# Kernel optimization log

Measured on AMD Instinct MI355X. Metric: run time of the kernel, lower is better.

The kernel has to match this reference:

```python
import jax, jax.numpy as jnp
import numpy as np

N = 50000
E = 800000
D_IN, D_HID, D_OUT = 128, 128, 128
BN_EPS = 1e-5


def gcn_conv(x, W, b, src, dst, n_nodes):
    # PyG GCNConv: add self-loops, symmetric normalization, scatter-add aggregation.
    loop = jnp.arange(n_nodes)
    s = jnp.concatenate([src, loop])
    d = jnp.concatenate([dst, loop])
    w = jnp.ones(s.shape[0], x.dtype)
    deg = jax.ops.segment_sum(w, d, num_segments=n_nodes)
    dinv = jnp.where(deg > 0, jax.lax.rsqrt(deg), 0.0)
    norm = dinv[s] * w * dinv[d]            # [E+N]
    h = x @ W                                # [N, d_out]
    msg = norm[:, None] * h[s]               # gather + scale
    out = jax.ops.segment_sum(msg, d, num_segments=n_nodes)
    return out + b


def batchnorm_prelu(x, gamma, beta, alpha):
    # BatchNorm1d in training mode (batch statistics, biased variance) + PReLU.
    mu = jnp.mean(x, axis=0)
    var = jnp.mean(jnp.square(x - mu), axis=0)
    y = (x - mu) * jax.lax.rsqrt(var + BN_EPS) * gamma + beta
    return jnp.where(y > 0, y, alpha * y)


def setup_inputs() -> dict:
    key = jax.random.key(0)
    ks = jax.random.split(key, 4)
    x = jax.random.normal(ks[0], (N, D_IN), dtype=jnp.float32)
    edge_index = jax.random.randint(ks[1], (2, E), 0, N, dtype=jnp.int64)
    s1 = 1.0 / np.sqrt(D_IN)
    s2 = 1.0 / np.sqrt(D_HID)
    W1 = jax.random.uniform(ks[2], (D_IN, D_HID), jnp.float32, -s1, s1)
    W2 = jax.random.uniform(ks[3], (D_HID, D_OUT), jnp.float32, -s2, s2)
    return {
        "x": x,
        "edge_index": edge_index,
        "W1": W1, "b1": jnp.zeros((D_HID,), jnp.float32),
        "g1": jnp.ones((D_HID,), jnp.float32), "be1": jnp.zeros((D_HID,), jnp.float32),
        "a1": jnp.full((1,), 0.25, jnp.float32),
        "W2": W2, "b2": jnp.zeros((D_OUT,), jnp.float32),
        "g2": jnp.ones((D_OUT,), jnp.float32), "be2": jnp.zeros((D_OUT,), jnp.float32),
        "a2": jnp.full((1,), 0.25, jnp.float32),
    }


def reference(x, edge_index, W1, b1, g1, be1, a1, W2, b2, g2, be2, a2):
    src, dst = edge_index[0], edge_index[1]
    h = gcn_conv(x, W1, b1, src, dst, N)
    h = batchnorm_prelu(h, g1, be1, a1)
    h = gcn_conv(h, W2, b2, src, dst, N)
    h = batchnorm_prelu(h, g2, be2, a2)
    return h
```

## Files before the change

kernel.cpp:

```cpp
#include <hip/hip_runtime.h>
#include <hip/hip_bf16.h>


typedef __hip_bfloat16 bf16;
typedef __attribute__((ext_vector_type(8))) short short8;
typedef __attribute__((ext_vector_type(4))) float f32x4;

#define NN 50000
#define NE 800000
#define DD 128
#define BN_EPS 1e-5f
#define BIN_CHUNK 3125
#define CAP 18432
#define NBKT 49

__device__ __forceinline__ float b2f(bf16 v) { return __bfloat162float(v); }
__device__ __forceinline__ float ldf(const void* p, size_t idx, int isbf) {
  return isbf ? b2f(((const bf16*)p)[idx]) : ((const float*)p)[idx];
}
__device__ __forceinline__ int lde(const void* ei, size_t idx, int is64) {
  return is64 ? (int)((const long long*)ei)[idx] : ((const int*)ei)[idx];
}
__device__ __forceinline__ unsigned int f2bs(float v) {
  bf16 b = __float2bfloat16(v);
  return (unsigned int)*reinterpret_cast<unsigned short*>(&b);
}
__device__ __forceinline__ float bslo(unsigned int u) { return __uint_as_float(u << 16); }
__device__ __forceinline__ float bshi(unsigned int u) { return __uint_as_float(u & 0xFFFF0000u); }
__device__ __forceinline__ float s2f(short v) {
  return __uint_as_float(((unsigned int)(unsigned short)v) << 16);
}

__global__ __launch_bounds__(256) void k_bin(const int* ei_i, const unsigned short* x16,
                                             const void* W1, const void* W2,
                                             unsigned short* wp1, unsigned short* wp2,
                                             int* flags, int* tailc, unsigned int* binned) {
  __shared__ int cnt[64], cur[64], gb[64], sflags[2];
  __shared__ unsigned int ebuf[BIN_CHUNK];
  const int tid = threadIdx.x;
  const int bid = blockIdx.x;
  if (tid < 64) {
    unsigned long long m1 = __ballot(ei_i[2 * tid + 1] != 0);
    int ex = (x16[2 * tid] >> 7) & 0xFF;
    unsigned long long m2 = __ballot(ex >= 90 && ex <= 140);
    if (tid == 0) {
      sflags[0] = (m1 == 0ull) ? 1 : 0;
      sflags[1] = (__popcll(m2) >= 48) ? 1 : 0;
    }
    cnt[tid] = 0;
    cur[tid] = 0;
  }
  __syncthreads();
  const int is64 = sflags[0], isbf = sflags[1];
  if (bid == 0 && tid == 0) { flags[0] = is64; flags[1] = isbf; }
  if (bid < 128) {
    const void* W = bid < 64 ? W1 : W2;
    unsigned short* wp = bid < 64 ? wp1 : wp2;
    int idx = (bid & 63) * 256 + tid;
    int k = idx >> 7, n = idx & 127;
    wp[(k >> 3) * 1024 + n * 8 + (k & 7)] = (unsigned short)f2bs(ldf(W, idx, isbf));
  }
  const void* ei = (const void*)ei_i;
  const int e0 = bid * BIN_CHUNK;
  for (int t = tid; t < BIN_CHUNK; t += 256) {
    int s = lde(ei, (size_t)(e0 + t), is64);
    int d = lde(ei, (size_t)NE + e0 + t, is64);
    ebuf[t] = ((unsigned)s << 16) | ((unsigned)(d >> 10) << 10) | (unsigned)(d & 1023);
    atomicAdd(&cnt[d >> 10], 1);
  }
  __syncthreads();
  if (tid < 64 && cnt[tid] > 0) gb[tid] = tid * CAP + atomicAdd(&tailc[tid], cnt[tid]);
  __syncthreads();
  for (int t = tid; t < BIN_CHUNK; t += 256) {
    unsigned int u = ebuf[t];
    int b = (int)((u >> 10) & 63);
    int r = atomicAdd(&cur[b], 1);
    binned[gb[b] + r] = u;
  }
}

__global__ __launch_bounds__(1024) void k_degfill(const unsigned int* binned, const int* tailc,
                                                  float* dinv, int* rowptr, int* rowend,
                                                  int* csr_src) {
  __shared__ int hist[1024];
  const int b = blockIdx.x;
  const int t = threadIdx.x;
  hist[t] = 0;
  __syncthreads();
  const int eb = b * CAP, ee = eb + tailc[b];
  for (int e = eb + t; e < ee; e += 1024) atomicAdd(&hist[binned[e] & 1023], 1);
  __syncthreads();
  int h = hist[t];
  __syncthreads();
  for (int off = 1; off < 1024; off <<= 1) {
    int u = (t >= off) ? hist[t - off] : 0;
    __syncthreads();
    hist[t] += u;
    __syncthreads();
  }
  int start = eb + hist[t] - h;
  int node = b * 1024 + t;
  if (node < NN) {
    rowptr[node] = start;
    rowend[node] = start + h;
    dinv[node] = rsqrtf((float)(h + 1));
  }
  __syncthreads();
  hist[t] = start;
  __syncthreads();
  for (int e = eb + t; e < ee; e += 1024) {
    unsigned int u = binned[e];
    int pos = atomicAdd(&hist[u & 1023], 1);
    csr_src[pos] = (int)(u >> 16);
  }
}

template <int XMODE>
__global__ __launch_bounds__(256) void k_gemm(const void* in_, const unsigned short* wp,
                                              const int* flags, const float* dinv,
                                              const float* statsp, const void* g,
                                              const void* be, const void* al,
                                              float* zstats, unsigned int* out) {
  __shared__ alignas(16) short sW[16 * 128 * 8];
  __shared__ float sSc[DD], sSh[DD], sAl;
  const int isbf = flags[1];
  const int tid = threadIdx.x;

  if (blockIdx.x < 64) zstats[blockIdx.x * 256 + tid] = 0.f;
  {
    const short8* src = (const short8*)wp;
    short8* dst = (short8*)sW;
#pragma unroll
    for (int i = 0; i < 8; i++) dst[tid + i * 256] = src[tid + i * 256];
  }
  if (XMODE == 2) {
    if (tid < DD) {
      float s = 0.f, q = 0.f;
#pragma unroll 8
      for (int k = 0; k < 64; k++) {
        s += statsp[k * 256 + tid];
        q += statsp[k * 256 + 128 + tid];
      }
      const float inv_n = 1.0f / NN;
      float mu = s * inv_n;
      float var = q * inv_n - mu * mu;
      float sc = rsqrtf(var + BN_EPS) * ldf(g, tid, isbf);
      sSc[tid] = sc;
      sSh[tid] = ldf(be, tid, isbf) - mu * sc;
    }
    if (tid == 0) sAl = ldf(al, 0, isbf);
  }
  __syncthreads();

  const int wave = tid >> 6;
  const int lane = tid & 63;
  const int quad = lane >> 4;
  const int m16 = lane & 15;
  const int r0 = blockIdx.x * 128 + wave * 32;

  f32x4 acc[2][8];
#pragma unroll
  for (int t = 0; t < 2; t++)
#pragma unroll
    for (int n = 0; n < 8; n++) acc[t][n] = (f32x4){0.f, 0.f, 0.f, 0.f};

#pragma unroll
  for (int q = 0; q < 4; q++) {
    const int kq = q * 32 + quad * 8;
    short8 af[2];
#pragma unroll
    for (int t = 0; t < 2; t++) {
      int row = r0 + t * 16 + m16;
      row = row < NN ? row : NN - 1;
      if (XMODE == 2) {
        short8 raw = *(const short8*)((const short*)in_ + (size_t)row * DD + kq);
        short8 f;
#pragma unroll
        for (int jj = 0; jj < 8; jj++) {
          float y = s2f(raw[jj]);
          y = y * sSc[kq + jj] + sSh[kq + jj];
          y = y > 0.f ? y : sAl * y;
          f[jj] = (short)f2bs(y);
        }
        af[t] = f;
      } else if (isbf) {
        af[t] = *(const short8*)((const short*)in_ + (size_t)row * DD + kq);
      } else {
        const float* ap = (const float*)in_ + (size_t)row * DD + kq;
        const float4 u0 = *(const float4*)ap;
        const float4 u1 = *(const float4*)(ap + 4);
        float v[8] = {u0.x, u0.y, u0.z, u0.w, u1.x, u1.y, u1.z, u1.w};
        short8 f;
#pragma unroll
        for (int jj = 0; jj < 8; jj++) f[jj] = (short)f2bs(v[jj]);
        af[t] = f;
      }
    }
    const int c = q * 4 + quad;
    const short* bp = sW + c * 1024 + m16 * 8;
#pragma unroll
    for (int n = 0; n < 8; n++) {
      const short8 bfrag = *(const short8*)(bp + n * 128);
      acc[0][n] = __builtin_amdgcn_mfma_f32_16x16x32_bf16(af[0], bfrag, acc[0][n], 0, 0, 0);
      acc[1][n] = __builtin_amdgcn_mfma_f32_16x16x32_bf16(af[1], bfrag, acc[1][n], 0, 0, 0);
    }
  }

#pragma unroll
  for (int t = 0; t < 2; t++)
#pragma unroll
    for (int r = 0; r < 4; r++) {
      int row = r0 + t * 16 + quad * 4 + r;
      if (row < NN) {
        float di = dinv[row];
        unsigned int* orow = out + (size_t)row * 64;
#pragma unroll
        for (int n = 0; n < 4; n++) {
          unsigned int p = (f2bs(di * acc[t][n + 4][r]) << 16) | f2bs(di * acc[t][n][r]);
          orow[n * 16 + m16] = p;
        }
      }
    }
}

__global__ __launch_bounds__(256) void k_agg(const unsigned int* hs, const float* dinv,
                                             const int* rowptr, const int* rowend,
                                             const int* csr_src, const void* bias,
                                             const int* flags, unsigned short* out,
                                             float* statsp) {
  const int tid = threadIdx.x;
  int w = (blockIdx.x * 256 + tid) >> 6;
  int lane = tid & 63;
  float dd_ = dinv[w];
  unsigned int hv = hs[(size_t)w * 64 + lane];
  float ax = bslo(hv), ay = bshi(hv);
  int e = rowptr[w], e1 = rowend[w];
  for (; e + 7 < e1; e += 8) {
    int s0 = csr_src[e], s1 = csr_src[e + 1], s2 = csr_src[e + 2], s3 = csr_src[e + 3];
    int s4 = csr_src[e + 4], s5 = csr_src[e + 5], s6 = csr_src[e + 6], s7 = csr_src[e + 7];
    unsigned int v0 = hs[(size_t)s0 * 64 + lane];
    unsigned int v1 = hs[(size_t)s1 * 64 + lane];
    unsigned int v2 = hs[(size_t)s2 * 64 + lane];
    unsigned int v3 = hs[(size_t)s3 * 64 + lane];
    unsigned int v4 = hs[(size_t)s4 * 64 + lane];
    unsigned int v5 = hs[(size_t)s5 * 64 + lane];
    unsigned int v6 = hs[(size_t)s6 * 64 + lane];
    unsigned int v7 = hs[(size_t)s7 * 64 + lane];
    ax += bslo(v0) + bslo(v1) + bslo(v2) + bslo(v3) + bslo(v4) + bslo(v5) + bslo(v6) + bslo(v7);
    ay += bshi(v0) + bshi(v1) + bshi(v2) + bshi(v3) + bshi(v4) + bshi(v5) + bshi(v6) + bshi(v7);
  }
  for (; e + 3 < e1; e += 4) {
    int s0 = csr_src[e], s1 = csr_src[e + 1], s2 = csr_src[e + 2], s3 = csr_src[e + 3];
    unsigned int v0 = hs[(size_t)s0 * 64 + lane];
    unsigned int v1 = hs[(size_t)s1 * 64 + lane];
    unsigned int v2 = hs[(size_t)s2 * 64 + lane];
    unsigned int v3 = hs[(size_t)s3 * 64 + lane];
    ax += bslo(v0) + bslo(v1) + bslo(v2) + bslo(v3);
    ay += bshi(v0) + bshi(v1) + bshi(v2) + bshi(v3);
  }
  for (; e < e1; e++) {
    unsigned int v0 = hs[(size_t)csr_src[e] * 64 + lane];
    ax += bslo(v0);
    ay += bshi(v0);
  }
  int isbf = flags[1];
  float o1 = dd_ * ax + ldf(bias, lane, isbf);
  float o2 = dd_ * ay + ldf(bias, lane + 64, isbf);
  unsigned short* orow = out + (size_t)w * DD;
  orow[lane] = (unsigned short)f2bs(o1);
  orow[lane + 64] = (unsigned short)f2bs(o2);

  __shared__ float rs1[256], rq1[256], rs2[256], rq2[256];
  rs1[tid] = o1; rq1[tid] = o1 * o1;
  rs2[tid] = o2; rq2[tid] = o2 * o2;
  __syncthreads();
  float* p = statsp + (blockIdx.x & 63) * 256;
  if (tid < 64) {
    float s = rs1[tid] + rs1[tid + 64] + rs1[tid + 128] + rs1[tid + 192];
    float q = rq1[tid] + rq1[tid + 64] + rq1[tid + 128] + rq1[tid + 192];
    atomicAdd(&p[tid], s);
    atomicAdd(&p[128 + tid], q);
  } else if (tid < 128) {
    int l = tid - 64;
    float s = rs2[l] + rs2[l + 64] + rs2[l + 128] + rs2[l + 192];
    float q = rq2[l] + rq2[l + 64] + rq2[l + 128] + rq2[l + 192];
    atomicAdd(&p[tid], s);
    atomicAdd(&p[128 + tid], q);
  }
}

__global__ __launch_bounds__(256) void k_bn_apply(const unsigned int* x32, const float* statsp,
                                                  const void* g, const void* be, const void* al,
                                                  const int* flags, void* out) {
  __shared__ float sSc[DD], sSh[DD], sAl;
  const int tid = threadIdx.x;
  const int isbf = flags[1];
  if (tid < DD) {
    float s = 0.f, q = 0.f;
#pragma unroll 8
    for (int k = 0; k < 64; k++) {
      s += statsp[k * 256 + tid];
      q += statsp[k * 256 + 128 + tid];
    }
    const float inv_n = 1.0f / NN;
    float mu = s * inv_n;
    float var = q * inv_n - mu * mu;
    float sc = rsqrtf(var + BN_EPS) * ldf(g, tid, isbf);
    sSc[tid] = sc;
    sSh[tid] = ldf(be, tid, isbf) - mu * sc;
  }
  if (tid == 0) sAl = ldf(al, 0, isbf);
  __syncthreads();
  const float alpha = sAl;
  for (int i4 = blockIdx.x * 256 + tid; i4 < NN * 32; i4 += gridDim.x * 256) {
    int jq = (i4 & 31) * 4;
    const uint2 xv = ((const uint2*)x32)[i4];
    float xa[4] = {bslo(xv.x), bshi(xv.x), bslo(xv.y), bshi(xv.y)};
    float y[4];
#pragma unroll
    for (int u = 0; u < 4; u++) {
      int j = jq + u;
      float v = xa[u] * sSc[j] + sSh[j];
      y[u] = v > 0.f ? v : alpha * v;
    }
    if (isbf) {
      uint2 o;
      o.x = (f2bs(y[1]) << 16) | f2bs(y[0]);
      o.y = (f2bs(y[3]) << 16) | f2bs(y[2]);
      ((uint2*)out)[i4] = o;
    } else {
      float4 o = {y[0], y[1], y[2], y[3]};
      ((float4*)out)[i4] = o;
    }
  }
}

extern "C" void kernel_launch(void* const* d_in, const int* in_sizes, int n_in,
                              void* d_out, int out_size, void* d_ws, size_t ws_size,
                              hipStream_t stream) {
  const void* x = d_in[0];
  const int* ei = (const int*)d_in[1];
  const void* W1 = d_in[2];
  const void* b1 = d_in[3];
  const void* g1 = d_in[4];
  const void* be1 = d_in[5];
  const void* a1 = d_in[6];
  const void* W2 = d_in[7];
  const void* b2 = d_in[8];
  const void* g2 = d_in[9];
  const void* be2 = d_in[10];
  const void* a2 = d_in[11];

  char* w = (char*)d_ws;
  float* dinv = (float*)w;
  int* flags = (int*)(w + 200704);
  int* rowptr = (int*)(w + 404800);
  int* rowend = (int*)(w + 604816);
  int* tailc = (int*)(w + 805632);
  float* stats1p = (float*)(w + 806400);
  float* stats2p = (float*)(w + 871936);
  int* csr_src = (int*)(w + 1048576);
  unsigned int* hbuf = (unsigned int*)(w + 4718592);
  unsigned short* wp1 = (unsigned short*)(w + 17518592);
  unsigned short* wp2 = (unsigned short*)(w + 17551360);
  unsigned short* aggbuf = (unsigned short*)(w + 30056448);
  unsigned int* binned = (unsigned int*)(w + 42856448);

  const int NB_G = (NN + 127) / 128;
  const int NB_W = NN * 64 / 256;

  hipMemsetAsync(tailc, 0, 256, stream);
  k_bin<<<dim3(256), dim3(256), 0, stream>>>(ei, (const unsigned short*)x, W1, W2,
                                             wp1, wp2, flags, tailc, binned);
  k_degfill<<<dim3(NBKT), dim3(1024), 0, stream>>>(binned, tailc, dinv, rowptr, rowend,
                                                   csr_src);

  k_gemm<0><<<dim3(NB_G), dim3(256), 0, stream>>>(x, wp1, flags, dinv,
                                                  nullptr, nullptr, nullptr, nullptr,
                                                  stats1p, hbuf);
  k_agg<<<dim3(NB_W), dim3(256), 0, stream>>>(hbuf, dinv, rowptr, rowend, csr_src,
                                              b1, flags, aggbuf, stats1p);

  k_gemm<2><<<dim3(NB_G), dim3(256), 0, stream>>>(aggbuf, wp2, flags, dinv,
                                                  stats1p, g1, be1, a1, stats2p, hbuf);
  k_agg<<<dim3(NB_W), dim3(256), 0, stream>>>(hbuf, dinv, rowptr, rowend, csr_src,
                                              b2, flags, aggbuf, stats2p);
  k_bn_apply<<<dim3(1024), dim3(256), 0, stream>>>((const unsigned int*)aggbuf, stats2p,
                                                   g2, be2, a2, flags, d_out);
}
```

Baseline: 240.0 us.

## Split hidden features into four column chunks for cache-resident aggregation

```diff
diff --git a/kernel.cpp b/kernel.cpp
--- a/kernel.cpp
+++ b/kernel.cpp
@@ -13,6 +13,8 @@
 #define BIN_CHUNK 3125
 #define CAP 18432
 #define NBKT 49
+#define CHS (NN * 16)
+#define NBAGG 12500
 
 __device__ __forceinline__ float b2f(bf16 v) { return __bfloat162float(v); }
 __device__ __forceinline__ float ldf(const void* p, size_t idx, int isbf) {
@@ -173,11 +175,17 @@
       int row = r0 + t * 16 + m16;
       row = row < NN ? row : NN - 1;
       if (XMODE == 2) {
-        short8 raw = *(const short8*)((const short*)in_ + (size_t)row * DD + kq);
+        const int s8 = kq & 63;
+        const unsigned int* pr = (const unsigned int*)in_ +
+            (size_t)(s8 >> 4) * CHS + (size_t)row * 16 + (s8 & 15);
+        const uint4 ra = *(const uint4*)pr;
+        const uint4 rb = *(const uint4*)(pr + 4);
+        unsigned int uu[8] = {ra.x, ra.y, ra.z, ra.w, rb.x, rb.y, rb.z, rb.w};
+        const bool hi = kq >= 64;
         short8 f;
 #pragma unroll
         for (int jj = 0; jj < 8; jj++) {
-          float y = s2f(raw[jj]);
+          float y = hi ? bshi(uu[jj]) : bslo(uu[jj]);
           y = y * sSc[kq + jj] + sSh[kq + jj];
           y = y > 0.f ? y : sAl * y;
           f[jj] = (short)f2bs(y);
@@ -213,11 +221,10 @@
       int row = r0 + t * 16 + quad * 4 + r;
       if (row < NN) {
         float di = dinv[row];
-        unsigned int* orow = out + (size_t)row * 64;
 #pragma unroll
         for (int n = 0; n < 4; n++) {
           unsigned int p = (f2bs(di * acc[t][n + 4][r]) << 16) | f2bs(di * acc[t][n][r]);
-          orow[n * 16 + m16] = p;
+          out[(size_t)n * CHS + (size_t)row * 16 + m16] = p;
         }
       }
     }
@@ -226,66 +233,78 @@
 __global__ __launch_bounds__(256) void k_agg(const unsigned int* hs, const float* dinv,
                                              const int* rowptr, const int* rowend,
                                              const int* csr_src, const void* bias,
-                                             const int* flags, unsigned short* out,
+                                             const int* flags, unsigned int* out,
                                              float* statsp) {
   const int tid = threadIdx.x;
-  int w = (blockIdx.x * 256 + tid) >> 6;
-  int lane = tid & 63;
-  float dd_ = dinv[w];
-  unsigned int hv = hs[(size_t)w * 64 + lane];
-  float ax = bslo(hv), ay = bshi(hv);
-  int e = rowptr[w], e1 = rowend[w];
-  for (; e + 7 < e1; e += 8) {
-    int s0 = csr_src[e], s1 = csr_src[e + 1], s2 = csr_src[e + 2], s3 = csr_src[e + 3];
-    int s4 = csr_src[e + 4], s5 = csr_src[e + 5], s6 = csr_src[e + 6], s7 = csr_src[e + 7];
-    unsigned int v0 = hs[(size_t)s0 * 64 + lane];
-    unsigned int v1 = hs[(size_t)s1 * 64 + lane];
-    unsigned int v2 = hs[(size_t)s2 * 64 + lane];
-    unsigned int v3 = hs[(size_t)s3 * 64 + lane];
-    unsigned int v4 = hs[(size_t)s4 * 64 + lane];
-    unsigned int v5 = hs[(size_t)s5 * 64 + lane];
-    unsigned int v6 = hs[(size_t)s6 * 64 + lane];
-    unsigned int v7 = hs[(size_t)s7 * 64 + lane];
-    ax += bslo(v0) + bslo(v1) + bslo(v2) + bslo(v3) + bslo(v4) + bslo(v5) + bslo(v6) + bslo(v7);
-    ay += bshi(v0) + bshi(v1) + bshi(v2) + bshi(v3) + bshi(v4) + bshi(v5) + bshi(v6) + bshi(v7);
-  }
-  for (; e + 3 < e1; e += 4) {
-    int s0 = csr_src[e], s1 = csr_src[e + 1], s2 = csr_src[e + 2], s3 = csr_src[e + 3];
-    unsigned int v0 = hs[(size_t)s0 * 64 + lane];
-    unsigned int v1 = hs[(size_t)s1 * 64 + lane];
-    unsigned int v2 = hs[(size_t)s2 * 64 + lane];
-    unsigned int v3 = hs[(size_t)s3 * 64 + lane];
+  const int c = blockIdx.x / NBAGG;
+  const int nb = blockIdx.x - c * NBAGG;
+  const int wave = tid >> 6;
+  const int lane = tid & 63;
+  const int grp = lane >> 4;
+  const int j = lane & 15;
+  const int w = nb * 4 + wave;
+  const unsigned int* hc = hs + (size_t)c * CHS;
+  const float dd_ = dinv[w];
+  unsigned int own = hc[(size_t)w * 16 + j];
+  float ax = 0.f, ay = 0.f;
+  if (grp == 0) { ax = bslo(own); ay = bshi(own); }
+  int e = rowptr[w];
+  const int e1 = rowend[w];
+  for (; e + 16 <= e1; e += 16) {
+    int s0 = csr_src[e + grp];
+    int s1 = csr_src[e + 4 + grp];
+    int s2 = csr_src[e + 8 + grp];
+    int s3 = csr_src[e + 12 + grp];
+    unsigned int v0 = hc[(size_t)s0 * 16 + j];
+    unsigned int v1 = hc[(size_t)s1 * 16 + j];
+    unsigned int v2 = hc[(size_t)s2 * 16 + j];
+    unsigned int v3 = hc[(size_t)s3 * 16 + j];
     ax += bslo(v0) + bslo(v1) + bslo(v2) + bslo(v3);
     ay += bshi(v0) + bshi(v1) + bshi(v2) + bshi(v3);
   }
-  for (; e < e1; e++) {
-    unsigned int v0 = hs[(size_t)csr_src[e] * 64 + lane];
+  for (; e + 8 <= e1; e += 8) {
+    int s0 = csr_src[e + grp];
+    int s1 = csr_src[e + 4 + grp];
+    unsigned int v0 = hc[(size_t)s0 * 16 + j];
+    unsigned int v1 = hc[(size_t)s1 * 16 + j];
+    ax += bslo(v0) + bslo(v1);
+    ay += bshi(v0) + bshi(v1);
+  }
+  if (e + 4 <= e1) {
+    int s0 = csr_src[e + grp];
+    unsigned int v0 = hc[(size_t)s0 * 16 + j];
     ax += bslo(v0);
     ay += bshi(v0);
-  }
-  int isbf = flags[1];
-  float o1 = dd_ * ax + ldf(bias, lane, isbf);
-  float o2 = dd_ * ay + ldf(bias, lane + 64, isbf);
-  unsigned short* orow = out + (size_t)w * DD;
-  orow[lane] = (unsigned short)f2bs(o1);
-  orow[lane + 64] = (unsigned short)f2bs(o2);
-
-  __shared__ float rs1[256], rq1[256], rs2[256], rq2[256];
-  rs1[tid] = o1; rq1[tid] = o1 * o1;
-  rs2[tid] = o2; rq2[tid] = o2 * o2;
-  __syncthreads();
-  float* p = statsp + (blockIdx.x & 63) * 256;
+    e += 4;
+  }
+  if (grp < e1 - e) {
+    unsigned int v0 = hc[(size_t)csr_src[e + grp] * 16 + j];
+    ax += bslo(v0);
+    ay += bshi(v0);
+  }
+  ax += __shfl_xor(ax, 16);
+  ax += __shfl_xor(ax, 32);
+  ay += __shfl_xor(ay, 16);
+  ay += __shfl_xor(ay, 32);
+  const int isbf = flags[1];
+  const int col1 = c * 16 + j;
+  const float o1 = dd_ * ax + ldf(bias, col1, isbf);
+  const float o2 = dd_ * ay + ldf(bias, col1 + 64, isbf);
+  __shared__ float red[4][4][16];
+  if (grp == 0) {
+    out[(size_t)c * CHS + (size_t)w * 16 + j] = (f2bs(o2) << 16) | f2bs(o1);
+    red[0][wave][j] = o1;
+    red[1][wave][j] = o1 * o1;
+    red[2][wave][j] = o2;
+    red[3][wave][j] = o2 * o2;
+  }
+  __syncthreads();
   if (tid < 64) {
-    float s = rs1[tid] + rs1[tid + 64] + rs1[tid + 128] + rs1[tid + 192];
-    float q = rq1[tid] + rq1[tid + 64] + rq1[tid + 128] + rq1[tid + 192];
-    atomicAdd(&p[tid], s);
-    atomicAdd(&p[128 + tid], q);
-  } else if (tid < 128) {
-    int l = tid - 64;
-    float s = rs2[l] + rs2[l + 64] + rs2[l + 128] + rs2[l + 192];
-    float q = rq2[l] + rq2[l + 64] + rq2[l + 128] + rq2[l + 192];
-    atomicAdd(&p[tid], s);
-    atomicAdd(&p[128 + tid], q);
+    const int st = tid >> 4, jj = tid & 15;
+    float v = red[st][0][jj] + red[st][1][jj] + red[st][2][jj] + red[st][3][jj];
+    const int col = (st >= 2 ? 64 : 0) + c * 16 + jj;
+    float* p = statsp + (blockIdx.x & 63) * 256;
+    atomicAdd(&p[col + ((st & 1) ? 128 : 0)], v);
   }
 }
 
@@ -312,25 +331,29 @@
   if (tid == 0) sAl = ldf(al, 0, isbf);
   __syncthreads();
   const float alpha = sAl;
-  for (int i4 = blockIdx.x * 256 + tid; i4 < NN * 32; i4 += gridDim.x * 256) {
-    int jq = (i4 & 31) * 4;
-    const uint2 xv = ((const uint2*)x32)[i4];
-    float xa[4] = {bslo(xv.x), bshi(xv.x), bslo(xv.y), bshi(xv.y)};
-    float y[4];
-#pragma unroll
-    for (int u = 0; u < 4; u++) {
-      int j = jq + u;
-      float v = xa[u] * sSc[j] + sSh[j];
-      y[u] = v > 0.f ? v : alpha * v;
-    }
+  for (int g2 = blockIdx.x * 256 + tid; g2 < NN * 32; g2 += gridDim.x * 256) {
+    const int c = g2 / (NN * 8);
+    const int rem = g2 - c * (NN * 8);
+    const int w = rem >> 3;
+    const int k = rem & 7;
+    const int j0 = c * 16 + k * 2;
+    const uint2 xv = ((const uint2*)x32)[g2];
+    float y0 = bslo(xv.x) * sSc[j0] + sSh[j0];
+    float y1 = bshi(xv.x) * sSc[j0 + 64] + sSh[j0 + 64];
+    float y2 = bslo(xv.y) * sSc[j0 + 1] + sSh[j0 + 1];
+    float y3 = bshi(xv.y) * sSc[j0 + 65] + sSh[j0 + 65];
+    y0 = y0 > 0.f ? y0 : alpha * y0;
+    y1 = y1 > 0.f ? y1 : alpha * y1;
+    y2 = y2 > 0.f ? y2 : alpha * y2;
+    y3 = y3 > 0.f ? y3 : alpha * y3;
     if (isbf) {
-      uint2 o;
-      o.x = (f2bs(y[1]) << 16) | f2bs(y[0]);
-      o.y = (f2bs(y[3]) << 16) | f2bs(y[2]);
-      ((uint2*)out)[i4] = o;
+      ((unsigned int*)out)[(size_t)w * 64 + (j0 >> 1)] = (f2bs(y2) << 16) | f2bs(y0);
+      ((unsigned int*)out)[(size_t)w * 64 + 32 + (j0 >> 1)] = (f2bs(y3) << 16) | f2bs(y1);
     } else {
-      float4 o = {y[0], y[1], y[2], y[3]};
-      ((float4*)out)[i4] = o;
+      float2 lo = {y0, y2};
+      float2 hi = {y1, y3};
+      ((float2*)out)[(size_t)w * 64 + (j0 >> 1)] = lo;
+      ((float2*)out)[(size_t)w * 64 + 32 + (j0 >> 1)] = hi;
     }
   }
 }
@@ -363,11 +386,10 @@
   unsigned int* hbuf = (unsigned int*)(w + 4718592);
   unsigned short* wp1 = (unsigned short*)(w + 17518592);
   unsigned short* wp2 = (unsigned short*)(w + 17551360);
-  unsigned short* aggbuf = (unsigned short*)(w + 30056448);
+  unsigned int* aggbuf = (unsigned int*)(w + 30056448);
   unsigned int* binned = (unsigned int*)(w + 42856448);
 
   const int NB_G = (NN + 127) / 128;
-  const int NB_W = NN * 64 / 256;
 
   hipMemsetAsync(tailc, 0, 256, stream);
   k_bin<<<dim3(256), dim3(256), 0, stream>>>(ei, (const unsigned short*)x, W1, W2,
@@ -378,13 +400,13 @@
   k_gemm<0><<<dim3(NB_G), dim3(256), 0, stream>>>(x, wp1, flags, dinv,
                                                   nullptr, nullptr, nullptr, nullptr,
                                                   stats1p, hbuf);
-  k_agg<<<dim3(NB_W), dim3(256), 0, stream>>>(hbuf, dinv, rowptr, rowend, csr_src,
-                                              b1, flags, aggbuf, stats1p);
+  k_agg<<<dim3(4 * NBAGG), dim3(256), 0, stream>>>(hbuf, dinv, rowptr, rowend, csr_src,
+                                                   b1, flags, aggbuf, stats1p);
 
   k_gemm<2><<<dim3(NB_G), dim3(256), 0, stream>>>(aggbuf, wp2, flags, dinv,
                                                   stats1p, g1, be1, a1, stats2p, hbuf);
-  k_agg<<<dim3(NB_W), dim3(256), 0, stream>>>(hbuf, dinv, rowptr, rowend, csr_src,
-                                              b2, flags, aggbuf, stats2p);
-  k_bn_apply<<<dim3(1024), dim3(256), 0, stream>>>((const unsigned int*)aggbuf, stats2p,
+  k_agg<<<dim3(4 * NBAGG), dim3(256), 0, stream>>>(hbuf, dinv, rowptr, rowend, csr_src,
+                                                   b2, flags, aggbuf, stats2p);
+  k_bn_apply<<<dim3(1024), dim3(256), 0, stream>>>(aggbuf, stats2p,
                                                    g2, be2, a2, flags, d_out);
 }
```

After: 329.5 us. 1.37x slower.

## Vectorize GCN aggregation gather with 16-byte loads across four edge groups

Applied to the files above, without the earlier changes.

```diff
diff --git a/kernel.cpp b/kernel.cpp
--- a/kernel.cpp
+++ b/kernel.cpp
@@ -229,63 +229,109 @@
                                              const int* flags, unsigned short* out,
                                              float* statsp) {
   const int tid = threadIdx.x;
-  int w = (blockIdx.x * 256 + tid) >> 6;
-  int lane = tid & 63;
-  float dd_ = dinv[w];
-  unsigned int hv = hs[(size_t)w * 64 + lane];
-  float ax = bslo(hv), ay = bshi(hv);
-  int e = rowptr[w], e1 = rowend[w];
-  for (; e + 7 < e1; e += 8) {
-    int s0 = csr_src[e], s1 = csr_src[e + 1], s2 = csr_src[e + 2], s3 = csr_src[e + 3];
-    int s4 = csr_src[e + 4], s5 = csr_src[e + 5], s6 = csr_src[e + 6], s7 = csr_src[e + 7];
-    unsigned int v0 = hs[(size_t)s0 * 64 + lane];
-    unsigned int v1 = hs[(size_t)s1 * 64 + lane];
-    unsigned int v2 = hs[(size_t)s2 * 64 + lane];
-    unsigned int v3 = hs[(size_t)s3 * 64 + lane];
-    unsigned int v4 = hs[(size_t)s4 * 64 + lane];
-    unsigned int v5 = hs[(size_t)s5 * 64 + lane];
-    unsigned int v6 = hs[(size_t)s6 * 64 + lane];
-    unsigned int v7 = hs[(size_t)s7 * 64 + lane];
-    ax += bslo(v0) + bslo(v1) + bslo(v2) + bslo(v3) + bslo(v4) + bslo(v5) + bslo(v6) + bslo(v7);
-    ay += bshi(v0) + bshi(v1) + bshi(v2) + bshi(v3) + bshi(v4) + bshi(v5) + bshi(v6) + bshi(v7);
-  }
-  for (; e + 3 < e1; e += 4) {
-    int s0 = csr_src[e], s1 = csr_src[e + 1], s2 = csr_src[e + 2], s3 = csr_src[e + 3];
-    unsigned int v0 = hs[(size_t)s0 * 64 + lane];
-    unsigned int v1 = hs[(size_t)s1 * 64 + lane];
-    unsigned int v2 = hs[(size_t)s2 * 64 + lane];
-    unsigned int v3 = hs[(size_t)s3 * 64 + lane];
-    ax += bslo(v0) + bslo(v1) + bslo(v2) + bslo(v3);
-    ay += bshi(v0) + bshi(v1) + bshi(v2) + bshi(v3);
-  }
-  for (; e < e1; e++) {
-    unsigned int v0 = hs[(size_t)csr_src[e] * 64 + lane];
-    ax += bslo(v0);
-    ay += bshi(v0);
-  }
-  int isbf = flags[1];
-  float o1 = dd_ * ax + ldf(bias, lane, isbf);
-  float o2 = dd_ * ay + ldf(bias, lane + 64, isbf);
-  unsigned short* orow = out + (size_t)w * DD;
-  orow[lane] = (unsigned short)f2bs(o1);
-  orow[lane + 64] = (unsigned short)f2bs(o2);
-
-  __shared__ float rs1[256], rq1[256], rs2[256], rq2[256];
-  rs1[tid] = o1; rq1[tid] = o1 * o1;
-  rs2[tid] = o2; rq2[tid] = o2 * o2;
-  __syncthreads();
-  float* p = statsp + (blockIdx.x & 63) * 256;
-  if (tid < 64) {
-    float s = rs1[tid] + rs1[tid + 64] + rs1[tid + 128] + rs1[tid + 192];
-    float q = rq1[tid] + rq1[tid + 64] + rq1[tid + 128] + rq1[tid + 192];
-    atomicAdd(&p[tid], s);
-    atomicAdd(&p[128 + tid], q);
-  } else if (tid < 128) {
-    int l = tid - 64;
-    float s = rs2[l] + rs2[l + 64] + rs2[l + 128] + rs2[l + 192];
-    float q = rq2[l] + rq2[l + 64] + rq2[l + 128] + rq2[l + 192];
-    atomicAdd(&p[tid], s);
-    atomicAdd(&p[128 + tid], q);
+  const int w = (blockIdx.x * 256 + tid) >> 6;
+  const int lane = tid & 63;
+  const int grp = lane >> 4;
+  const int j = lane & 15;
+  const uint4* hs4 = (const uint4*)hs;
+  const float dd_ = dinv[w];
+  const int isbf = flags[1];
+
+  float ax[4] = {0.f, 0.f, 0.f, 0.f};
+  float ay[4] = {0.f, 0.f, 0.f, 0.f};
+  if (grp == 0) {
+    const uint4 own = hs4[(size_t)w * 16 + j];
+    ax[0] = bslo(own.x); ay[0] = bshi(own.x);
+    ax[1] = bslo(own.y); ay[1] = bshi(own.y);
+    ax[2] = bslo(own.z); ay[2] = bshi(own.z);
+    ax[3] = bslo(own.w); ay[3] = bshi(own.w);
+  }
+
+#define ACC4(v)                                              \
+  do {                                                       \
+    ax[0] += bslo((v).x); ay[0] += bshi((v).x);              \
+    ax[1] += bslo((v).y); ay[1] += bshi((v).y);              \
+    ax[2] += bslo((v).z); ay[2] += bshi((v).z);              \
+    ax[3] += bslo((v).w); ay[3] += bshi((v).w);              \
+  } while (0)
+
+  int e = rowptr[w];
+  const int e1 = rowend[w];
+  for (; e + 16 <= e1; e += 16) {
+    const int s0 = __builtin_nontemporal_load(&csr_src[e + grp]);
+    const int s1 = __builtin_nontemporal_load(&csr_src[e + 4 + grp]);
+    const int s2 = __builtin_nontemporal_load(&csr_src[e + 8 + grp]);
+    const int s3 = __builtin_nontemporal_load(&csr_src[e + 12 + grp]);
+    const uint4 v0 = hs4[(size_t)s0 * 16 + j];
+    const uint4 v1 = hs4[(size_t)s1 * 16 + j];
+    const uint4 v2 = hs4[(size_t)s2 * 16 + j];
+    const uint4 v3 = hs4[(size_t)s3 * 16 + j];
+    ACC4(v0); ACC4(v1); ACC4(v2); ACC4(v3);
+  }
+  for (; e + 8 <= e1; e += 8) {
+    const int s0 = __builtin_nontemporal_load(&csr_src[e + grp]);
+    const int s1 = __builtin_nontemporal_load(&csr_src[e + 4 + grp]);
+    const uint4 v0 = hs4[(size_t)s0 * 16 + j];
+    const uint4 v1 = hs4[(size_t)s1 * 16 + j];
+    ACC4(v0); ACC4(v1);
+  }
+  if (e + 4 <= e1) {
+    const int s0 = __builtin_nontemporal_load(&csr_src[e + grp]);
+    const uint4 v0 = hs4[(size_t)s0 * 16 + j];
+    ACC4(v0);
+    e += 4;
+  }
+  if (grp < e1 - e) {
+    const int s0 = __builtin_nontemporal_load(&csr_src[e + grp]);
+    const uint4 v0 = hs4[(size_t)s0 * 16 + j];
+    ACC4(v0);
+  }
+#undef ACC4
+
+#pragma unroll
+  for (int u = 0; u < 4; u++) {
+    ax[u] += __shfl_xor(ax[u], 16);
+    ax[u] += __shfl_xor(ax[u], 32);
+    ay[u] += __shfl_xor(ay[u], 16);
+    ay[u] += __shfl_xor(ay[u], 32);
+  }
+
+  float o1[4], o2[4];
+#pragma unroll
+  for (int u = 0; u < 4; u++) {
+    const int cc = 4 * j + u;
+    o1[u] = dd_ * ax[u] + ldf(bias, cc, isbf);
+    o2[u] = dd_ * ay[u] + ldf(bias, cc + 64, isbf);
+  }
+
+  __shared__ float rs1[4][64], rq1[4][64], rs2[4][64], rq2[4][64];
+  const int wv = tid >> 6;
+  if (grp == 0) {
+    unsigned long long p1 =
+        ((unsigned long long)((f2bs(o1[3]) << 16) | f2bs(o1[2])) << 32) |
+        (unsigned long long)((f2bs(o1[1]) << 16) | f2bs(o1[0]));
+    unsigned long long p2 =
+        ((unsigned long long)((f2bs(o2[3]) << 16) | f2bs(o2[2])) << 32) |
+        (unsigned long long)((f2bs(o2[1]) << 16) | f2bs(o2[0]));
+    unsigned long long* o64 = (unsigned long long*)(out + (size_t)w * DD);
+    __builtin_nontemporal_store(p1, &o64[j]);
+    __builtin_nontemporal_store(p2, &o64[16 + j]);
+#pragma unroll
+    for (int u = 0; u < 4; u++) {
+      rs1[wv][4 * j + u] = o1[u];
+      rq1[wv][4 * j + u] = o1[u] * o1[u];
+      rs2[wv][4 * j + u] = o2[u];
+      rq2[wv][4 * j + u] = o2[u] * o2[u];
+    }
+  }
+  __syncthreads();
+  {
+    const int col = tid & 63, sel = tid >> 6;
+    const float* rr = sel == 0 ? &rs1[0][0] : sel == 1 ? &rs2[0][0]
+                    : sel == 2 ? &rq1[0][0] : &rq2[0][0];
+    const float v = rr[col] + rr[64 + col] + rr[128 + col] + rr[192 + col];
+    float* p = statsp + (blockIdx.x & 63) * 256;
+    atomicAdd(&p[sel * 64 + col], v);
   }
 }
 
```

New measurement: 263.1 us. +9.6%, slower.
